# Kernel tuning notes

Hardware: AMD Instinct MI355X
Metric: run time of the kernel (lower is better)

## Reference

```python
import jax, jax.numpy as jnp
import numpy as np

B, T, D = 2, 2048, 1024
K, F = 8, 4096
LAMBDA = 0.5


def setup_inputs() -> dict:
    key = jax.random.key(0)
    ks = jax.random.split(key, 8)
    s = 0.02
    return {
        "x": jax.random.normal(ks[0], (B, T, D), dtype=jnp.float32),
        "prev_logits": jax.random.normal(ks[1], (B, T, K), dtype=jnp.float32),
        "Wt": jax.random.normal(ks[2], (D, K), dtype=jnp.float32) * s,
        "Wgt": jax.random.normal(ks[3], (K, K), dtype=jnp.float32) * s,
        "We_logits": jnp.zeros((K,), dtype=jnp.float32),
        "W1": jax.random.normal(ks[4], (K, D, F), dtype=jnp.float32) * s,
        "b1": jnp.zeros((K, F), dtype=jnp.float32),
        "W2": jax.random.normal(ks[5], (K, F, D), dtype=jnp.float32) * s,
        "b2": jnp.zeros((K, D), dtype=jnp.float32),
    }


def reference(x, prev_logits, Wt, Wgt, We_logits, W1, b1, W2, b2):
    # gating: softmax over router logits, sigmoid-threshold multi-hot mask
    logits = jnp.einsum("btd,dk->btk", x, Wt) + jnp.einsum("btk,kj->btj", prev_logits, Wgt)
    st = jax.nn.softmax(logits, axis=-1)                       # (B,T,K)
    We = jax.nn.sigmoid(We_logits)                             # (K,)
    mask = (st > LAMBDA * We).astype(x.dtype)                  # (B,T,K)
    g = st * mask
    sel_counts = mask.sum(axis=(0, 1))                         # (K,)
    avg_density = mask.sum(axis=-1).mean()                     # scalar

    # dense multi-expert FFN: every expert on every token (dropout=0 / eval)
    h = jax.nn.gelu(jnp.einsum("btd,kdf->bktf", x, W1) + b1[:, None, :], approximate=False)
    outk = jnp.einsum("bktf,kfd->bktd", h, W2) + b2[:, None, :]  # (B,K,T,D)
    y = jnp.einsum("btk,bktd->btd", g, outk)
    y = y / (g.sum(axis=-1, keepdims=True) + 1e-6)
    return y, jax.lax.stop_gradient(logits), sel_counts, avg_density
```

## Files before the change

kernel.cpp:

```cpp
#include <hip/hip_runtime.h>
#include <cstdint>
#include <cstddef>

#define NB 2
#define NTT 2048
#define ND 1024
#define NK 8
#define NF 4096
#define NTOK (NB*NTT)
#define LAMBDA_C 0.5f

#define Y_SZ   (NTOK*ND)
#define LG_OFF Y_SZ
#define SC_OFF (LG_OFF + NTOK*NK)
#define AD_OFF (SC_OFF + NK)

#define WS_CNT    0
#define WS_SEG    8
#define WS_NTILES 17
#define WS_TILEK  32
#define WS_TILER  1056
#define WS_PTOK   4096
#define WS_PCOEF  36864
#define WS_COEF   69632
#define WS_X16    102400
#define WS_H      2199552

#define BM 128
#define BN 64
#define BK 64
#define SPLITK2 4
#define KT 16

#define AOFF0 0u
#define AOFF1 16384u
#define BOFF0 32768u
#define BOFF1 40960u

typedef float  f32x4 __attribute__((ext_vector_type(4)));
typedef _Float16 f16x8 __attribute__((ext_vector_type(8)));
typedef unsigned int u32x2 __attribute__((ext_vector_type(2)));
typedef unsigned int u32x4 __attribute__((ext_vector_type(4)));

__device__ __forceinline__ unsigned int pkrtz(float a, float b){
    auto h = __builtin_amdgcn_cvt_pkrtz(a, b);
    return __builtin_bit_cast(unsigned int, h);
}
__device__ __forceinline__ float gelu_exact(float v){
    return 0.5f * v * (1.0f + erff(v * 0.70710678118654752440f));
}

__global__ __launch_bounds__(256) void k_xcast(const float* __restrict__ x,
                                               unsigned short* __restrict__ x16)
{
    int i = (blockIdx.x*256 + threadIdx.x) * 16;
    const f32x4* src = (const f32x4*)(x + i);
    f32x4 v0 = src[0], v1 = src[1], v2 = src[2], v3 = src[3];
    u32x4 o0 = {pkrtz(v0[0],v0[1]), pkrtz(v0[2],v0[3]), pkrtz(v1[0],v1[1]), pkrtz(v1[2],v1[3])};
    u32x4 o1 = {pkrtz(v2[0],v2[1]), pkrtz(v2[2],v2[3]), pkrtz(v3[0],v3[1]), pkrtz(v3[2],v3[3])};
    *(u32x4*)(x16 + i)     = o0;
    *(u32x4*)(x16 + i + 8) = o1;
}

__global__ __launch_bounds__(256) void k_gating(
    const float* __restrict__ x, const float* __restrict__ pl,
    const float* __restrict__ Wt, const float* __restrict__ Wgt,
    const float* __restrict__ Wel, float* __restrict__ out,
    float* __restrict__ coef, int* __restrict__ cnt)
{
    int t = blockIdx.x;
    const float* xt = x + (size_t)t * ND;
    float acc[NK] = {0,0,0,0,0,0,0,0};
    for (int d = threadIdx.x; d < ND; d += 256){
        float xv = xt[d];
        const float4* w = (const float4*)(Wt + (size_t)d * NK);
        float4 w0 = w[0], w1 = w[1];
        acc[0] += xv*w0.x; acc[1] += xv*w0.y; acc[2] += xv*w0.z; acc[3] += xv*w0.w;
        acc[4] += xv*w1.x; acc[5] += xv*w1.y; acc[6] += xv*w1.z; acc[7] += xv*w1.w;
    }
    __shared__ float red[4][NK];
    #pragma unroll
    for (int k = 0; k < NK; k++){
        float v = acc[k];
        #pragma unroll
        for (int off = 32; off; off >>= 1) v += __shfl_down(v, off);
        if ((threadIdx.x & 63) == 0) red[threadIdx.x >> 6][k] = v;
    }
    __syncthreads();
    if (threadIdx.x == 0){
        const float* p = pl + (size_t)t * NK;
        float pv[NK];
        #pragma unroll
        for (int j = 0; j < NK; j++) pv[j] = p[j];
        float lg[NK]; float mx = -1e30f;
        #pragma unroll
        for (int k = 0; k < NK; k++){
            float v = red[0][k] + red[1][k] + red[2][k] + red[3][k];
            #pragma unroll
            for (int j = 0; j < NK; j++) v += pv[j] * Wgt[j*NK + k];
            lg[k] = v; mx = fmaxf(mx, v);
            out[LG_OFF + (size_t)t*NK + k] = v;
        }
        float e[NK]; float s = 0.f;
        #pragma unroll
        for (int k = 0; k < NK; k++){ e[k] = expf(lg[k] - mx); s += e[k]; }
        float g[NK]; float gsum = 0.f;
        #pragma unroll
        for (int k = 0; k < NK; k++){
            float st = e[k] / s;
            float we = 1.f / (1.f + expf(-Wel[k]));
            bool m = st > LAMBDA_C * we;
            g[k] = m ? st : 0.f;
            gsum += g[k];
        }
        float inv = 1.f / (gsum + 1e-6f);
        #pragma unroll
        for (int k = 0; k < NK; k++){
            coef[(size_t)t*NK + k] = g[k] * inv;
            if (g[k] > 0.f) atomicAdd(&cnt[k], 1);
        }
    }
}

__global__ __launch_bounds__(256) void k_scan(
    const float* __restrict__ coef, int* __restrict__ wsi,
    float* __restrict__ wsf, int pair_cap)
{
    int k = blockIdx.x;
    const int* cnt = wsi + WS_CNT;
    int base = 0;
    for (int j = 0; j < k; j++) base += cnt[j];
    int tid = threadIdx.x, lane = tid & 63, w = tid >> 6;
    __shared__ int wsum[4];
    __shared__ int sbase;
    if (tid == 0){
        sbase = base;
        wsi[WS_SEG + k] = base;
        if (k == NK-1) wsi[WS_SEG + NK] = base + cnt[k];
    }
    __syncthreads();
    int* ptok = wsi + WS_PTOK;
    float* pc = wsf + WS_PCOEF;
    for (int c0 = 0; c0 < NTOK; c0 += 256){
        int t = c0 + tid;
        float c = coef[(size_t)t*NK + k];
        bool m = c > 0.f;
        unsigned long long bal = __ballot(m);
        int pre = __popcll(bal & ((1ull << lane) - 1ull));
        if (lane == 0) wsum[w] = __popcll(bal);
        __syncthreads();
        int b = sbase;
        for (int j = 0; j < w; j++) b += wsum[j];
        if (m){
            int pos = b + pre;
            if (pos < pair_cap){ ptok[pos] = t; pc[pos] = c; }
        }
        __syncthreads();
        if (tid == 0) sbase += wsum[0] + wsum[1] + wsum[2] + wsum[3];
        __syncthreads();
    }
}

__global__ void k_tiles(int* __restrict__ wsi, float* __restrict__ out, int pair_cap)
{
    if (threadIdx.x == 0 && blockIdx.x == 0){
        const int* cnt = wsi + WS_CNT;
        const int* seg = wsi + WS_SEG;
        int total = 0;
        for (int k = 0; k < NK; k++){ total += cnt[k]; out[SC_OFF + k] = (float)cnt[k]; }
        out[AD_OFF] = (float)total / (float)NTOK;
        int nt = 0;
        for (int k = 0; k < NK; k++){
            int e = min(seg[k+1], pair_cap);
            for (int r = seg[k]; r < e; r += BM){
                wsi[WS_TILEK + nt] = k; wsi[WS_TILER + nt] = r; nt++;
            }
        }
        wsi[WS_NTILES] = nt;
    }
}

#define XCD_PART_LOOP(nwork)                                              \
    int q_ = (nwork) >> 3, rr_ = (nwork) & 7;                             \
    int xcd_ = blockIdx.x & 7;                                            \
    int slot_ = blockIdx.x >> 3;                                          \
    int nslot_ = gridDim.x >> 3;                                          \
    int cntw_ = q_ + (xcd_ < rr_ ? 1 : 0);                                \
    int start_ = xcd_ * q_ + (xcd_ < rr_ ? xcd_ : rr_);                   \
    for (int p_ = slot_; p_ < cntw_; p_ += nslot_)


#define LOAD_A(dst_, tt_)                                                 \
    { const unsigned short* an_ = asrc + (tt_)*BK;                        \
      _Pragma("unroll")                                                   \
      for (int j_ = 0; j_ < 4; j_++) dst_[j_] = *(const u32x4*)(an_ + j_*8); }

#define LOAD_B(dst_, tt_, LDW_)                                           \
    { const float* bn_ = bsrc + (size_t)((tt_)*BK + bkq*4)*LDW_;          \
      _Pragma("unroll")                                                   \
      for (int r_ = 0; r_ < 4; r_++) dst_[r_] = *(const f32x4*)(bn_ + (size_t)r_*LDW_); }

#define STAGE_A(src_, AO_)                                                \
    { _Pragma("unroll")                                                   \
      for (int j_ = 0; j_ < 4; j_++){                                     \
          unsigned off_ = (AO_) + (unsigned)arow*128u +                   \
              ((((unsigned)(ahalf*4 + j_)) ^ (unsigned)(arow & 7)) << 4); \
          *(u32x4*)(&lds[off_]) = src_[j_];                               \
      } }

#define STAGE_B(src_, BO_)                                                \
    { unsigned wA_[4], wB_[4];                                            \
      _Pragma("unroll")                                                   \
      for (int r_ = 0; r_ < 4; r_++){                                     \
          wA_[r_] = pkrtz(src_[r_][0], src_[r_][1]);                      \
          wB_[r_] = pkrtz(src_[r_][2], src_[r_][3]);                      \
      }                                                                   \
      _Pragma("unroll")                                                   \
      for (int j_ = 0; j_ < 4; j_++){                                     \
          unsigned s0_ = (j_ < 2) ? wA_[1] : wB_[1];                      \
          unsigned s1_ = (j_ < 2) ? wA_[0] : wB_[0];                      \
          unsigned s2_ = (j_ < 2) ? wA_[3] : wB_[3];                      \
          unsigned s3_ = (j_ < 2) ? wA_[2] : wB_[2];                      \
          unsigned sel_ = (j_ & 1) ? 0x07060302u : 0x05040100u;           \
          unsigned o0_ = __builtin_amdgcn_perm(s0_, s1_, sel_);           \
          unsigned o1_ = __builtin_amdgcn_perm(s2_, s3_, sel_);           \
          unsigned col_ = (unsigned)(bcc*4 + j_);                         \
          unsigned off_ = (BO_) + col_*128u +                             \
              (((unsigned)(bkq*8)) ^ ((col_ & 7u) << 4));                 \
          *(u32x2*)(&lds[off_]) = (u32x2){o0_, o1_};                      \
      } }

#define MFMA_RD(AO_, BO_)                                                 \
    { __builtin_amdgcn_s_setprio(1);                                      \
      _Pragma("unroll")                                                   \
      for (int kk_ = 0; kk_ < 2; kk_++){                                  \
          unsigned sb_ = ((unsigned)(kk_*64 + q*16)) ^ swzL;              \
          f16x8 af_[4], bf_[2];                                           \
          _Pragma("unroll")                                               \
          for (int m_ = 0; m_ < 4; m_++)                                  \
              af_[m_] = *(const f16x8*)(&lds[(AO_) + (unsigned)(wr*64 + m_*16 + l15)*128u + sb_]); \
          _Pragma("unroll")                                               \
          for (int n_ = 0; n_ < 2; n_++)                                  \
              bf_[n_] = *(const f16x8*)(&lds[(BO_) + (unsigned)(wc*32 + n_*16 + l15)*128u + sb_]); \
          _Pragma("unroll")                                               \
          for (int m_ = 0; m_ < 4; m_++)                                  \
          _Pragma("unroll")                                               \
          for (int n_ = 0; n_ < 2; n_++)                                  \
              acc[m_][n_] = __builtin_amdgcn_mfma_f32_16x16x32_f16(af_[m_], bf_[n_], acc[m_][n_], 0, 0, 0); \
      }                                                                   \
      __builtin_amdgcn_s_setprio(0); }

#define STEP_SYNC()                                                       \
    asm volatile("s_waitcnt lgkmcnt(0)" ::: "memory");                    \
    __builtin_amdgcn_s_barrier();                                         \
    __builtin_amdgcn_sched_barrier(0);

__global__ __launch_bounds__(256, 3) void k_gemm1(
    const unsigned short* __restrict__ x16, const float* __restrict__ W1,
    const float* __restrict__ b1, const int* __restrict__ wsi,
    unsigned short* __restrict__ hbuf, int pair_cap)
{
    __shared__ char lds[49152];
    __shared__ int stok[BM];
    const int* seg  = wsi + WS_SEG;
    const int* tk   = wsi + WS_TILEK;
    const int* tr   = wsi + WS_TILER;
    const int* ptok = wsi + WS_PTOK;
    int ntm = wsi[WS_NTILES];
    int nwork = ntm * (NF / BN);
    int tid  = threadIdx.x;
    int lane = tid & 63;
    int w    = tid >> 6;
    int wr = w >> 1, wc = w & 1;
    int l15 = lane & 15, q = lane >> 4;
    unsigned swzL = (unsigned)((l15 & 7) << 4);
    int arow = tid >> 1, ahalf = tid & 1;
    int bkq = tid >> 4, bcc = tid & 15;

    XCD_PART_LOOP(nwork){
        int widx = start_ + p_;
        int mt = widx % ntm;
        int ft = widx / ntm;
        int kexp = tk[mt];
        int row0 = tr[mt];
        int nrows = min(BM, seg[kexp+1] - row0);
        int f0 = ft * BN;
        __syncthreads();
        if (tid < BM){
            int r = row0 + tid;
            stok[tid] = (tid < nrows && r < pair_cap) ? ptok[r] : ptok[row0];
        }
        __syncthreads();
        const unsigned short* asrc = x16 + (size_t)stok[arow]*ND + ahalf*32;
        const float* bsrc = W1 + (size_t)kexp*ND*NF + f0 + bcc*4;
        u32x4 ga0[4], ga1[4]; f32x4 gb0[4], gb1[4];
        LOAD_A(ga0, 0) LOAD_B(gb0, 0, NF)
        LOAD_A(ga1, 1) LOAD_B(gb1, 1, NF)
        f32x4 acc[4][2] = {};
        for (int t = 0; t < KT; t += 2){
            STAGE_A(ga0, AOFF0) STAGE_B(gb0, BOFF0)
            if (t + 2 < KT){ LOAD_A(ga0, t+2) LOAD_B(gb0, t+2, NF) }
            STEP_SYNC()
            MFMA_RD(AOFF0, BOFF0)
            STAGE_A(ga1, AOFF1) STAGE_B(gb1, BOFF1)
            if (t + 3 < KT){ LOAD_A(ga1, t+3) LOAD_B(gb1, t+3, NF) }
            STEP_SYNC()
            MFMA_RD(AOFF1, BOFF1)
        }
        const float* b1k = b1 + (size_t)kexp*NF;
        #pragma unroll
        for (int n = 0; n < 2; n++){
            int f = f0 + wc*32 + n*16 + l15;
            float bv = b1k[f];
            #pragma unroll
            for (int m = 0; m < 4; m++){
                int rl = wr*64 + m*16 + q*4;
                #pragma unroll
                for (int i = 0; i < 4; i++){
                    int r = rl + i;
                    if (r < nrows && row0 + r < pair_cap){
                        float v = gelu_exact(acc[m][n][i] + bv);
                        hbuf[(size_t)(row0+r)*NF + f] = (unsigned short)(pkrtz(v, 0.f) & 0xffffu);
                    }
                }
            }
        }
    }
}

__global__ __launch_bounds__(256, 3) void k_gemm2(
    const unsigned short* __restrict__ hbuf, const float* __restrict__ W2,
    const float* __restrict__ b2, const int* __restrict__ wsi,
    const float* __restrict__ wsf, float* __restrict__ out, int pair_cap)
{
    __shared__ char lds[49152];
    __shared__ int stok[BM];
    __shared__ float scoef[BM];
    const int* seg  = wsi + WS_SEG;
    const int* tk   = wsi + WS_TILEK;
    const int* tr   = wsi + WS_TILER;
    const int* ptok = wsi + WS_PTOK;
    const float* pcoef = wsf + WS_PCOEF;
    int ntm = wsi[WS_NTILES];
    int nwork = ntm * (ND / BN) * SPLITK2;
    int tid  = threadIdx.x;
    int lane = tid & 63;
    int w    = tid >> 6;
    int wr = w >> 1, wc = w & 1;
    int l15 = lane & 15, q = lane >> 4;
    unsigned swzL = (unsigned)((l15 & 7) << 4);
    int arow = tid >> 1, ahalf = tid & 1;
    int bkq = tid >> 4, bcc = tid & 15;

    XCD_PART_LOOP(nwork){
        int widx = start_ + p_;
        int mt = widx % ntm;
        int rest = widx / ntm;
        int dt = rest & 15;
        int sp = rest >> 4;
        int kexp = tk[mt];
        int row0 = tr[mt];
        int nrows = min(BM, seg[kexp+1] - row0);
        int d0 = dt * BN;
        __syncthreads();
        if (tid < BM){
            int r = row0 + tid;
            bool v = (tid < nrows && r < pair_cap);
            stok[tid]  = v ? ptok[r] : 0;
            scoef[tid] = v ? pcoef[r] : 0.f;
        }
        __syncthreads();
        int hr = row0 + arow; if (hr >= pair_cap) hr = pair_cap - 1;
        const unsigned short* asrc = hbuf + (size_t)hr*NF + sp*(NF/SPLITK2) + ahalf*32;
        const float* bsrc = W2 + (size_t)kexp*NF*ND + (size_t)sp*(NF/SPLITK2)*ND + d0 + bcc*4;
        u32x4 ga0[4], ga1[4]; f32x4 gb0[4], gb1[4];
        LOAD_A(ga0, 0) LOAD_B(gb0, 0, ND)
        LOAD_A(ga1, 1) LOAD_B(gb1, 1, ND)
        f32x4 acc[4][2] = {};
        for (int t = 0; t < KT; t += 2){
            STAGE_A(ga0, AOFF0) STAGE_B(gb0, BOFF0)
            if (t + 2 < KT){ LOAD_A(ga0, t+2) LOAD_B(gb0, t+2, ND) }
            STEP_SYNC()
            MFMA_RD(AOFF0, BOFF0)
            STAGE_A(ga1, AOFF1) STAGE_B(gb1, BOFF1)
            if (t + 3 < KT){ LOAD_A(ga1, t+3) LOAD_B(gb1, t+3, ND) }
            STEP_SYNC()
            MFMA_RD(AOFF1, BOFF1)
        }
        const float* b2k = b2 + (size_t)kexp*ND;
        #pragma unroll
        for (int n = 0; n < 2; n++){
            int d = d0 + wc*32 + n*16 + l15;
            float bv = (sp == 0) ? b2k[d] : 0.f;
            #pragma unroll
            for (int m = 0; m < 4; m++){
                int rl = wr*64 + m*16 + q*4;
                #pragma unroll
                for (int i = 0; i < 4; i++){
                    int r = rl + i;
                    if (r < nrows && row0 + r < pair_cap){
                        float c = scoef[r];
                        atomicAdd(&out[(size_t)stok[r]*ND + d], c * (acc[m][n][i] + bv));
                    }
                }
            }
        }
    }
}

extern "C" void kernel_launch(void* const* d_in, const int* in_sizes, int n_in,
                              void* d_out, int out_size, void* d_ws, size_t ws_size,
                              hipStream_t stream)
{
    const float* x   = (const float*)d_in[0];
    const float* pl  = (const float*)d_in[1];
    const float* Wt  = (const float*)d_in[2];
    const float* Wgt = (const float*)d_in[3];
    const float* Wel = (const float*)d_in[4];
    const float* W1  = (const float*)d_in[5];
    const float* b1  = (const float*)d_in[6];
    const float* W2  = (const float*)d_in[7];
    const float* b2  = (const float*)d_in[8];
    float* out = (float*)d_out;
    int* wsi   = (int*)d_ws;
    float* wsf = (float*)d_ws;
    unsigned short* x16  = (unsigned short*)((char*)d_ws + (size_t)WS_X16*4);
    unsigned short* hbuf = (unsigned short*)((char*)d_ws + (size_t)WS_H*4);

    long long avail = (long long)ws_size - (long long)WS_H*4;
    long long cap = avail / ((long long)NF*2);
    if (cap > (long long)NTOK*NK) cap = (long long)NTOK*NK;
    if (cap < 0) cap = 0;
    int pair_cap = (int)cap;

    hipMemsetAsync(d_out, 0, (size_t)out_size*sizeof(float), stream);
    hipMemsetAsync(d_ws, 0, 32, stream);
    k_xcast<<<1024, 256, 0, stream>>>(x, x16);
    k_gating<<<NTOK, 256, 0, stream>>>(x, pl, Wt, Wgt, Wel, out, wsf + WS_COEF, wsi + WS_CNT);
    if (pair_cap > 0){
        k_scan<<<NK, 256, 0, stream>>>(wsf + WS_COEF, wsi, wsf, pair_cap);
        k_tiles<<<1, 64, 0, stream>>>(wsi, out, pair_cap);
        k_gemm1<<<2048, 256, 0, stream>>>(x16, W1, b1, wsi, hbuf, pair_cap);
        k_gemm2<<<2048, 256, 0, stream>>>(hbuf, W2, b2, wsi, wsf, out, pair_cap);
    }
}
```

Measured before the change: 244.4 us.

## Pre-transpose expert weights to fp16 and use async-LDS 128x128 GEMM kernels

Adds a kernel that converts W1 and W2 to fp16 and transposes them into workspace on every call. Both expert GEMMs are rewritten to use global_load_lds direct-to-LDS double buffering, a 128x128 output tile, a swizzled K-major layout and occupancy 4. The goal is to halve the weight bytes each GEMM streams and to remove the in-loop fp32-to-fp16 conversion and register staging. In exchange, every call pays a full pass that reads all fp32 weights and writes the fp16 copies. The new path needs a much larger workspace and falls back to the old kernels when the workspace is too small.

```diff
diff --git a/kernel.cpp b/kernel.cpp
--- a/kernel.cpp
+++ b/kernel.cpp
@@ -24,7 +24,11 @@
 #define WS_PCOEF  36864
 #define WS_COEF   69632
 #define WS_X16    102400
-#define WS_H      2199552
+#define B_X16   409600ull
+#define B_W1T   8798208ull
+#define B_W2T   75907072ull
+#define B_HBUFN 143015936ull
+#define B_HBUFF 8798208ull
 
 #define BM 128
 #define BN 64
@@ -60,6 +64,54 @@
     u32x4 o1 = {pkrtz(v2[0],v2[1]), pkrtz(v2[2],v2[3]), pkrtz(v3[0],v3[1]), pkrtz(v3[2],v3[3])};
     *(u32x4*)(x16 + i)     = o0;
     *(u32x4*)(x16 + i + 8) = o1;
+}
+
+__global__ __launch_bounds__(256) void k_wtrans(
+    const float* __restrict__ W1, const float* __restrict__ W2,
+    unsigned short* __restrict__ W1T, unsigned short* __restrict__ W2T)
+{
+    __shared__ unsigned short LT[64][72];
+    int b = blockIdx.x;
+    const float* src; unsigned short* dst; int sld, dld;
+    if (b < 8192){
+        int k = b >> 10, dt = (b >> 6) & 15, ft = b & 63;
+        src = W1 + ((size_t)k*ND + dt*64)*NF + ft*64; sld = NF;
+        dst = W1T + ((size_t)k*NF + ft*64)*ND + dt*64; dld = ND;
+    } else {
+        int b2 = b - 8192;
+        int k = b2 >> 10, ft = (b2 >> 4) & 63, dt = b2 & 15;
+        src = W2 + ((size_t)k*NF + ft*64)*ND + dt*64; sld = ND;
+        dst = W2T + ((size_t)k*ND + dt*64)*NF + ft*64; dld = NF;
+    }
+    int t = threadIdx.x;
+    int rg = t >> 4, cg = t & 15;
+    f32x4 v[4];
+    #pragma unroll
+    for (int i = 0; i < 4; i++) v[i] = *(const f32x4*)(src + (size_t)(rg*4+i)*sld + cg*4);
+    unsigned wA[4], wB[4];
+    #pragma unroll
+    for (int r = 0; r < 4; r++){
+        wA[r] = pkrtz(v[r][0], v[r][1]);
+        wB[r] = pkrtz(v[r][2], v[r][3]);
+    }
+    #pragma unroll
+    for (int j = 0; j < 4; j++){
+        unsigned s0 = (j < 2) ? wA[1] : wB[1];
+        unsigned s1 = (j < 2) ? wA[0] : wB[0];
+        unsigned s2 = (j < 2) ? wA[3] : wB[3];
+        unsigned s3 = (j < 2) ? wA[2] : wB[2];
+        unsigned sel = (j & 1) ? 0x07060302u : 0x05040100u;
+        unsigned o0 = __builtin_amdgcn_perm(s0, s1, sel);
+        unsigned o1 = __builtin_amdgcn_perm(s2, s3, sel);
+        *(u32x2*)(&LT[cg*4+j][rg*4]) = (u32x2){o0, o1};
+    }
+    __syncthreads();
+    int c = t >> 2, ch = t & 3;
+    u32x4 r0 = *(const u32x4*)(&LT[c][ch*16]);
+    u32x4 r1 = *(const u32x4*)(&LT[c][ch*16 + 8]);
+    unsigned short* dp = dst + (size_t)c*dld + ch*16;
+    *(u32x4*)(dp)     = r0;
+    *(u32x4*)(dp + 8) = r1;
 }
 
 __global__ __launch_bounds__(256) void k_gating(
@@ -189,6 +241,191 @@
     int start_ = xcd_ * q_ + (xcd_ < rr_ ? xcd_ : rr_);                   \
     for (int p_ = slot_; p_ < cntw_; p_ += nslot_)
 
+
+#define GLLN(aP0_, aP1_, bP0_, bP1_, t_, slot_)                           \
+  { unsigned ab_ = (unsigned)(slot_)*16384u + (unsigned)(wv*1024);        \
+    __builtin_amdgcn_global_load_lds(                                     \
+        (const __attribute__((address_space(1))) void*)((aP0_) + (size_t)(t_)*32), \
+        (__attribute__((address_space(3))) void*)(&lds[ab_]), 16, 0, 0);  \
+    __builtin_amdgcn_global_load_lds(                                     \
+        (const __attribute__((address_space(1))) void*)((aP1_) + (size_t)(t_)*32), \
+        (__attribute__((address_space(3))) void*)(&lds[ab_ + 4096u]), 16, 0, 0); \
+    __builtin_amdgcn_global_load_lds(                                     \
+        (const __attribute__((address_space(1))) void*)((bP0_) + (size_t)(t_)*32), \
+        (__attribute__((address_space(3))) void*)(&lds[ab_ + 8192u]), 16, 0, 0); \
+    __builtin_amdgcn_global_load_lds(                                     \
+        (const __attribute__((address_space(1))) void*)((bP1_) + (size_t)(t_)*32), \
+        (__attribute__((address_space(3))) void*)(&lds[ab_ + 12288u]), 16, 0, 0); }
+
+#define MFMAN(slot_)                                                      \
+  { unsigned ab_ = (unsigned)(slot_)*16384u, bb_ = ab_ + 8192u;           \
+    f16x8 af_[4], bf_[4];                                                 \
+    _Pragma("unroll")                                                     \
+    for (int m_ = 0; m_ < 4; m_++) af_[m_] = *(const f16x8*)(&lds[ab_ + aoff[m_]]); \
+    _Pragma("unroll")                                                     \
+    for (int n_ = 0; n_ < 4; n_++) bf_[n_] = *(const f16x8*)(&lds[bb_ + boff[n_]]); \
+    __builtin_amdgcn_s_setprio(1);                                        \
+    _Pragma("unroll")                                                     \
+    for (int m_ = 0; m_ < 4; m_++)                                        \
+    _Pragma("unroll")                                                     \
+    for (int n_ = 0; n_ < 4; n_++)                                        \
+        acc[m_][n_] = __builtin_amdgcn_mfma_f32_16x16x32_f16(af_[m_], bf_[n_], acc[m_][n_], 0, 0, 0); \
+    __builtin_amdgcn_s_setprio(0); }
+
+#define GEMMN_PRE()                                                       \
+    int tid = threadIdx.x;                                                \
+    int L = tid & 63;                                                     \
+    int wv = tid >> 6;                                                    \
+    int wr = wv >> 1, wc = wv & 1;                                        \
+    int l15 = L & 15, q = L >> 4;                                         \
+    unsigned aoff[4], boff[4];                                            \
+    _Pragma("unroll")                                                     \
+    for (int m_ = 0; m_ < 4; m_++){                                       \
+        int r_ = wr*64 + m_*16 + l15;                                     \
+        aoff[m_] = (unsigned)(r_*64) + ((unsigned)((q ^ r_) & 3) << 4);   \
+    }                                                                     \
+    _Pragma("unroll")                                                     \
+    for (int n_ = 0; n_ < 4; n_++){                                       \
+        int c_ = wc*64 + n_*16 + l15;                                     \
+        boff[n_] = (unsigned)(c_*64) + ((unsigned)((q ^ c_) & 3) << 4);   \
+    }                                                                     \
+    int grow0 = wv*16 + (L >> 2);                                         \
+    int grow1 = (4 + wv)*16 + (L >> 2);                                   \
+    int qg8 = (((L & 3) ^ ((L >> 2) & 3))) * 8;
+
+__global__ __launch_bounds__(256, 4) void k_gemm1n(
+    const unsigned short* __restrict__ x16, const unsigned short* __restrict__ w1t,
+    const float* __restrict__ b1, const int* __restrict__ wsi,
+    unsigned short* __restrict__ hbuf, int pair_cap)
+{
+    __shared__ char lds[32768];
+    __shared__ int stok[BM];
+    const int* seg  = wsi + WS_SEG;
+    const int* tk   = wsi + WS_TILEK;
+    const int* tr   = wsi + WS_TILER;
+    const int* ptok = wsi + WS_PTOK;
+    int ntm = wsi[WS_NTILES];
+    int nwork = ntm * (NF / 128);
+    GEMMN_PRE()
+
+    XCD_PART_LOOP(nwork){
+        int widx = start_ + p_;
+        int mt = widx % ntm;
+        int ft = widx / ntm;
+        int kexp = tk[mt];
+        int row0 = tr[mt];
+        int nrows = min(BM, seg[kexp+1] - row0);
+        int f0 = ft * 128;
+        __syncthreads();
+        if (tid < BM){
+            int r = row0 + tid;
+            stok[tid] = (tid < nrows && r < pair_cap) ? ptok[r] : ptok[row0];
+        }
+        __syncthreads();
+        const unsigned short* a0 = x16 + (size_t)stok[grow0]*ND + qg8;
+        const unsigned short* a1 = x16 + (size_t)stok[grow1]*ND + qg8;
+        const unsigned short* bb = w1t + (size_t)kexp*NF*ND;
+        const unsigned short* b0 = bb + (size_t)(f0 + grow0)*ND + qg8;
+        const unsigned short* b1p = bb + (size_t)(f0 + grow1)*ND + qg8;
+        f32x4 acc[4][4] = {};
+        GLLN(a0, a1, b0, b1p, 0, 0)
+        __syncthreads();
+        for (int t = 0; t < 32; t++){
+            if (t + 1 < 32){ GLLN(a0, a1, b0, b1p, t+1, (t+1)&1) }
+            MFMAN(t & 1)
+            __syncthreads();
+        }
+        const float* b1k = b1 + (size_t)kexp*NF;
+        #pragma unroll
+        for (int n = 0; n < 4; n++){
+            int f = f0 + wc*64 + n*16 + l15;
+            float bv = b1k[f];
+            #pragma unroll
+            for (int m = 0; m < 4; m++){
+                int rl = wr*64 + m*16 + q*4;
+                #pragma unroll
+                for (int i = 0; i < 4; i++){
+                    int r = rl + i;
+                    if (r < nrows && row0 + r < pair_cap){
+                        float v = gelu_exact(acc[m][n][i] + bv);
+                        hbuf[(size_t)(row0+r)*NF + f] = (unsigned short)(pkrtz(v, 0.f) & 0xffffu);
+                    }
+                }
+            }
+        }
+    }
+}
+
+__global__ __launch_bounds__(256, 4) void k_gemm2n(
+    const unsigned short* __restrict__ hbuf, const unsigned short* __restrict__ w2t,
+    const float* __restrict__ b2, const int* __restrict__ wsi,
+    const float* __restrict__ wsf, float* __restrict__ out, int pair_cap)
+{
+    __shared__ char lds[32768];
+    __shared__ int stok[BM];
+    __shared__ float scoef[BM];
+    const int* seg  = wsi + WS_SEG;
+    const int* tk   = wsi + WS_TILEK;
+    const int* tr   = wsi + WS_TILER;
+    const int* ptok = wsi + WS_PTOK;
+    const float* pcoef = wsf + WS_PCOEF;
+    int ntm = wsi[WS_NTILES];
+    int nwork = ntm * (ND / 128) * SPLITK2;
+    GEMMN_PRE()
+
+    XCD_PART_LOOP(nwork){
+        int widx = start_ + p_;
+        int mt = widx % ntm;
+        int rest = widx / ntm;
+        int dt = rest & 7;
+        int spk = rest >> 3;
+        int kexp = tk[mt];
+        int row0 = tr[mt];
+        int nrows = min(BM, seg[kexp+1] - row0);
+        int d0 = dt * 128;
+        __syncthreads();
+        if (tid < BM){
+            int r = row0 + tid;
+            bool v = (tid < nrows && r < pair_cap);
+            stok[tid]  = v ? ptok[r] : 0;
+            scoef[tid] = v ? pcoef[r] : 0.f;
+        }
+        __syncthreads();
+        int ar0 = row0 + grow0; if (ar0 >= pair_cap) ar0 = pair_cap - 1;
+        int ar1 = row0 + grow1; if (ar1 >= pair_cap) ar1 = pair_cap - 1;
+        const unsigned short* a0 = hbuf + (size_t)ar0*NF + spk*(NF/SPLITK2) + qg8;
+        const unsigned short* a1 = hbuf + (size_t)ar1*NF + spk*(NF/SPLITK2) + qg8;
+        const unsigned short* bb = w2t + (size_t)kexp*ND*NF + spk*(NF/SPLITK2);
+        const unsigned short* b0 = bb + (size_t)(d0 + grow0)*NF + qg8;
+        const unsigned short* b1p = bb + (size_t)(d0 + grow1)*NF + qg8;
+        f32x4 acc[4][4] = {};
+        GLLN(a0, a1, b0, b1p, 0, 0)
+        __syncthreads();
+        for (int t = 0; t < 32; t++){
+            if (t + 1 < 32){ GLLN(a0, a1, b0, b1p, t+1, (t+1)&1) }
+            MFMAN(t & 1)
+            __syncthreads();
+        }
+        const float* b2k = b2 + (size_t)kexp*ND;
+        #pragma unroll
+        for (int n = 0; n < 4; n++){
+            int d = d0 + wc*64 + n*16 + l15;
+            float bv = (spk == 0) ? b2k[d] : 0.f;
+            #pragma unroll
+            for (int m = 0; m < 4; m++){
+                int rl = wr*64 + m*16 + q*4;
+                #pragma unroll
+                for (int i = 0; i < 4; i++){
+                    int r = rl + i;
+                    if (r < nrows && row0 + r < pair_cap){
+                        float c = scoef[r];
+                        atomicAdd(&out[(size_t)stok[r]*ND + d], c * (acc[m][n][i] + bv));
+                    }
+                }
+            }
+        }
+    }
+}
 
 #define LOAD_A(dst_, tt_)                                                 \
     { const unsigned short* an_ = asrc + (tt_)*BK;                        \
@@ -255,7 +492,7 @@
     __builtin_amdgcn_s_barrier();                                         \
     __builtin_amdgcn_sched_barrier(0);
 
-__global__ __launch_bounds__(256, 3) void k_gemm1(
+__global__ __launch_bounds__(256, 3) void k_gemm1f(
     const unsigned short* __restrict__ x16, const float* __restrict__ W1,
     const float* __restrict__ b1, const int* __restrict__ wsi,
     unsigned short* __restrict__ hbuf, int pair_cap)
@@ -328,7 +565,7 @@
     }
 }
 
-__global__ __launch_bounds__(256, 3) void k_gemm2(
+__global__ __launch_bounds__(256, 3) void k_gemm2f(
     const unsigned short* __restrict__ hbuf, const float* __restrict__ W2,
     const float* __restrict__ b2, const int* __restrict__ wsi,
     const float* __restrict__ wsf, float* __restrict__ out, int pair_cap)
@@ -424,23 +661,37 @@
     float* out = (float*)d_out;
     int* wsi   = (int*)d_ws;
     float* wsf = (float*)d_ws;
-    unsigned short* x16  = (unsigned short*)((char*)d_ws + (size_t)WS_X16*4);
-    unsigned short* hbuf = (unsigned short*)((char*)d_ws + (size_t)WS_H*4);
-
-    long long avail = (long long)ws_size - (long long)WS_H*4;
-    long long cap = avail / ((long long)NF*2);
-    if (cap > (long long)NTOK*NK) cap = (long long)NTOK*NK;
-    if (cap < 0) cap = 0;
-    int pair_cap = (int)cap;
+    unsigned short* x16 = (unsigned short*)((char*)d_ws + B_X16);
+
+    long long capn = ((long long)ws_size - (long long)B_HBUFN) / ((long long)NF*2);
+    bool newpath = capn >= 4096;
 
     hipMemsetAsync(d_out, 0, (size_t)out_size*sizeof(float), stream);
     hipMemsetAsync(d_ws, 0, 32, stream);
     k_xcast<<<1024, 256, 0, stream>>>(x, x16);
     k_gating<<<NTOK, 256, 0, stream>>>(x, pl, Wt, Wgt, Wel, out, wsf + WS_COEF, wsi + WS_CNT);
-    if (pair_cap > 0){
+
+    if (newpath){
+        unsigned short* w1t  = (unsigned short*)((char*)d_ws + B_W1T);
+        unsigned short* w2t  = (unsigned short*)((char*)d_ws + B_W2T);
+        unsigned short* hbuf = (unsigned short*)((char*)d_ws + B_HBUFN);
+        int pair_cap = (int)((capn > 32768) ? 32768 : capn);
+        k_wtrans<<<16384, 256, 0, stream>>>(W1, W2, w1t, w2t);
         k_scan<<<NK, 256, 0, stream>>>(wsf + WS_COEF, wsi, wsf, pair_cap);
         k_tiles<<<1, 64, 0, stream>>>(wsi, out, pair_cap);
-        k_gemm1<<<2048, 256, 0, stream>>>(x16, W1, b1, wsi, hbuf, pair_cap);
-        k_gemm2<<<2048, 256, 0, stream>>>(hbuf, W2, b2, wsi, wsf, out, pair_cap);
-    }
-}
+        k_gemm1n<<<2048, 256, 0, stream>>>(x16, w1t, b1, wsi, hbuf, pair_cap);
+        k_gemm2n<<<2048, 256, 0, stream>>>(hbuf, w2t, b2, wsi, wsf, out, pair_cap);
+    } else {
+        unsigned short* hbuf = (unsigned short*)((char*)d_ws + B_HBUFF);
+        long long cap = ((long long)ws_size - (long long)B_HBUFF) / ((long long)NF*2);
+        if (cap > (long long)NTOK*NK) cap = (long long)NTOK*NK;
+        if (cap < 0) cap = 0;
+        int pair_cap = (int)cap;
+        if (pair_cap > 0){
+            k_scan<<<NK, 256, 0, stream>>>(wsf + WS_COEF, wsi, wsf, pair_cap);
+            k_tiles<<<1, 64, 0, stream>>>(wsi, out, pair_cap);
+            k_gemm1f<<<2048, 256, 0, stream>>>(x16, W1, b1, wsi, hbuf, pair_cap);
+            k_gemm2f<<<2048, 256, 0, stream>>>(hbuf, W2, b2, wsi, wsf, out, pair_cap);
+        }
+    }
+}
```

Measured after the change: 269.9 us. +10.5%, slower.
